# Kernel tuning notes

Measured on AMD Instinct MI355X. Metric: run time of the kernel, lower is better.

Reference implementation:

```python
import jax, jax.numpy as jnp
import numpy as np

B = 131072
D_IN = 256
HID = 256
N_EXPERTS = 4
N_IN_CAPS = 1
CAP_DIM = 16
BN_EPS = 1e-5


def setup_inputs() -> dict:
    key = jax.random.key(0)
    ks = jax.random.split(key, 8)
    return {
        "x": jax.random.normal(ks[0], (B, D_IN), dtype=jnp.float32),
        "fc_w": jax.random.normal(ks[1], (HID, D_IN), dtype=jnp.float32) * (1.0 / np.sqrt(D_IN)),
        "fc_b": jax.random.normal(ks[2], (HID,), dtype=jnp.float32) * 0.01,
        "bn_gamma": jnp.ones((HID,), dtype=jnp.float32),
        "bn_beta": jnp.zeros((HID,), dtype=jnp.float32),
        "W_caps": jax.random.normal(ks[3], (N_EXPERTS, N_IN_CAPS, HID, CAP_DIM), dtype=jnp.float32),
        "out_w": jax.random.normal(ks[4], (N_EXPERTS, CAP_DIM), dtype=jnp.float32) * (1.0 / np.sqrt(CAP_DIM)),
        "out_b": jax.random.normal(ks[5], (N_EXPERTS,), dtype=jnp.float32) * 0.01,
    }


def _squash(v):
    # norm/(1+norm^2) * v/(norm+1e-8), norm over last axis
    norm = jnp.linalg.norm(v, axis=-1, keepdims=True)
    return (norm / (1.0 + norm * norm)) * (v / (norm + 1e-8))


def reference(x, fc_w, fc_b, bn_gamma, bn_beta, W_caps, out_w, out_b):
    # Linear 256->256
    h = x @ fc_w.T + fc_b                                   # [B, HID]
    # BatchNorm1d (training-mode batch statistics, biased variance)
    mean = jnp.mean(h, axis=0)
    var = jnp.mean(jnp.square(h - mean), axis=0)
    h = (h - mean) * jax.lax.rsqrt(var + BN_EPS) * bn_gamma + bn_beta
    h = jax.nn.relu(h)
    # Capsule layer: input capsules [B, N_IN, HID]
    x_cap = h[:, None, :]                                   # [B, 1, HID]
    # u[b,e,n,o] = sum_d x_cap[b,n,d] * W_caps[e,n,d,o]
    u = jnp.einsum('bnd,endo->beno', x_cap, W_caps)         # [B, E, 1, 16]
    u_hat = _squash(u)
    # dynamic routing, 3 iterations
    b = jnp.zeros((x.shape[0], N_EXPERTS, N_IN_CAPS), dtype=h.dtype)
    v = None
    for i in range(3):
        c = jax.nn.softmax(b, axis=1)                       # over experts
        s = jnp.sum(c[..., None] * u_hat, axis=2)           # [B, E, 16]
        v = _squash(s)
        if i < 2:
            b = b + jnp.sum(u_hat * v[:, :, None, :], axis=-1)
    # output head + softmax
    logits = jnp.einsum('bec,kc->bek', v, out_w) + out_b    # [B, E, E]
    return jax.nn.softmax(logits, axis=-1)
```

## Files before the change

### kernel.cpp

```cpp
#include <hip/hip_runtime.h>
#include <hip/hip_bf16.h>


#define BATCH   131072
#define INV_B   (1.0f / 131072.0f)

typedef __attribute__((ext_vector_type(8))) short  short8;
typedef __attribute__((ext_vector_type(4))) float  f32x4;

__device__ __forceinline__ unsigned bf16_rn(float f) {
    unsigned u = __float_as_uint(f);
    return (u + 0x7fffu + ((u >> 16) & 1u)) >> 16;
}

__device__ __forceinline__ unsigned pack2bf(float a, float b) {
    union { __hip_bfloat16 b; ushort u; } ca, cb;
    ca.b = __float2bfloat16(a);
    cb.b = __float2bfloat16(b);
    return (unsigned)ca.u | ((unsigned)cb.u << 16);
}

__device__ __forceinline__ void split8(const float* v, uint4& hi, uint4& lo) {
    unsigned hb[8], lb[8];
#pragma unroll
    for (int j = 0; j < 8; ++j) {
        union { __hip_bfloat16 b; ushort u; } ch, cl;
        ch.b = __float2bfloat16(v[j]);
        float res = v[j] - __bfloat162float(ch.b);
        cl.b = __float2bfloat16(res);
        hb[j] = ch.u;
        lb[j] = cl.u;
    }
    hi = make_uint4(hb[0] | (hb[1] << 16), hb[2] | (hb[3] << 16),
                    hb[4] | (hb[5] << 16), hb[6] | (hb[7] << 16));
    lo = make_uint4(lb[0] | (lb[1] << 16), lb[2] | (lb[3] << 16),
                    lb[4] | (lb[5] << 16), lb[6] | (lb[7] << 16));
}

__global__ void k_prep(const float* __restrict__ w, ushort* __restrict__ wsp,
                       float* __restrict__ gsum, float* __restrict__ gsq)
{
    if (blockIdx.x == 0) { gsum[threadIdx.x] = 0.f; gsq[threadIdx.x] = 0.f; }
    const int cid = (int)blockIdx.x * 256 + threadIdx.x;
    const int j   = cid >> 5;
    const int ks  = (cid >> 2) & 7;
    const int c   = cid & 3;
    const float* wp = w + j * 256 + ks * 32 + c * 8;
    float4 v0 = *(const float4*)(wp);
    float4 v1 = *(const float4*)(wp + 4);
    float va[8] = {v0.x, v0.y, v0.z, v0.w, v1.x, v1.y, v1.z, v1.w};
    uint4 hi, lo;
    split8(va, hi, lo);
    const int slot = (c + (j >> 1)) & 3;
    *(uint4*)&wsp[ks * 8192 + j * 32 + slot * 8]         = hi;
    *(uint4*)&wsp[65536 + ks * 8192 + j * 32 + slot * 8] = lo;
}

__global__ __launch_bounds__(256, 4) void k_gemm(
    const float* __restrict__ x, const ushort* __restrict__ wsp,
    const float* __restrict__ bias, ushort* __restrict__ h,
    float* __restrict__ gsum, float* __restrict__ gsq)
{
    __shared__ ushort POOL[16896];
    __shared__ float  csum[128];
    __shared__ float  csq[128];

    const int t   = threadIdx.x;
    const int wid = t >> 6;
    const int l   = t & 63;
    const int wm  = wid >> 1;
    const int wn  = wid & 1;
    const int g   = l >> 4;
    const int lc  = l & 15;

    const int wg = ((int)blockIdx.x & 7) * 256 + ((int)blockIdx.x >> 3);
    const int bm = (wg >> 1) * 128;
    const int bn = (wg & 1) * 128;

    if (t < 128) { csum[t] = 0.f; csq[t] = 0.f; }

    f32x4 acc[4][4];
#pragma unroll
    for (int mi = 0; mi < 4; ++mi)
#pragma unroll
        for (int ni = 0; ni < 4; ++ni)
            acc[mi][ni] = (f32x4){0.f, 0.f, 0.f, 0.f};

    float bb[4];
#pragma unroll
    for (int ni = 0; ni < 4; ++ni)
        bb[ni] = bias[bn + wn * 64 + ni * 16 + lc];

    const int arow = t >> 3;
    const int ac8  = t & 7;
    const int acp  = ac8 >> 1;
    const int ahf  = ac8 & 1;

    const int isLo    = wid >> 1;
    const int halfsel = wid & 1;

#pragma unroll 1
    for (int ks = 0; ks < 8; ++ks) {
        __syncthreads();

        {
            const char* src = (const char*)(wsp + isLo * 65536 + ks * 8192
                                            + bn * 32 + halfsel * 2048);
            char* dst = (char*)&POOL[4096 + isLo * 4096 + halfsel * 2048];
#pragma unroll
            for (int i = 0; i < 4; ++i) {
                __builtin_amdgcn_global_load_lds(
                    (const __attribute__((address_space(1))) unsigned*)(src + i * 1024 + l * 16),
                    (__attribute__((address_space(3))) unsigned*)(dst + i * 1024),
                    16, 0, 0);
            }
        }

#pragma unroll
        for (int p = 0; p < 4; ++p) {
            const int r = p * 32 + arow;
            const float* ap = x + (size_t)(bm + r) * 256 + ks * 32 + ac8 * 4;
            float4 v = *(const float4*)ap;
            uint2 pk;
            pk.x = pack2bf(v.x, v.y);
            pk.y = pack2bf(v.z, v.w);
            const int s = (acp + (r >> 1)) & 3;
            *(uint2*)&POOL[r * 32 + s * 8 + ahf * 4] = pk;
        }
        __syncthreads();

        short8 ahfrag[4];
#pragma unroll
        for (int mi = 0; mi < 4; ++mi) {
            const int row = wm * 64 + mi * 16 + lc;
            const int off = row * 32 + ((g + (row >> 1)) & 3) * 8;
            ahfrag[mi] = *(const short8*)&POOL[off];
        }
#pragma unroll
        for (int ni = 0; ni < 4; ++ni) {
            const int col = wn * 64 + ni * 16 + lc;
            const int off = col * 32 + ((g + (col >> 1)) & 3) * 8;
            short8 bhf = *(const short8*)&POOL[4096 + off];
            short8 blf = *(const short8*)&POOL[8192 + off];
#pragma unroll
            for (int mi = 0; mi < 4; ++mi) {
                acc[mi][ni] = __builtin_amdgcn_mfma_f32_16x16x32_bf16(
                    ahfrag[mi], bhf, acc[mi][ni], 0, 0, 0);
                acc[mi][ni] = __builtin_amdgcn_mfma_f32_16x16x32_bf16(
                    ahfrag[mi], blf, acc[mi][ni], 0, 0, 0);
            }
        }
    }

    __syncthreads();

    float lsum[4] = {0.f, 0.f, 0.f, 0.f};
    float lsq[4]  = {0.f, 0.f, 0.f, 0.f};

#pragma unroll
    for (int mi = 0; mi < 4; ++mi)
#pragma unroll
        for (int ni = 0; ni < 4; ++ni) {
            const int colL = wn * 64 + ni * 16 + lc;
#pragma unroll
            for (int reg = 0; reg < 4; ++reg) {
                const int rowL = wm * 64 + mi * 16 + g * 4 + reg;
                float hv = acc[mi][ni][reg] + bb[ni];
                unsigned hb = bf16_rn(hv);
                float hq = __uint_as_float(hb << 16);
                POOL[rowL * 132 + colL] = (ushort)hb;
                lsum[ni] += hq;
                lsq[ni]   = fmaf(hq, hq, lsq[ni]);
            }
        }
    __syncthreads();

#pragma unroll
    for (int p = 0; p < 8; ++p) {
        const int r   = p * 16 + (t >> 4);
        const int c16 = t & 15;
        short8 vv = *(const short8*)&POOL[r * 132 + c16 * 8];
        *(short8*)(h + (size_t)(bm + r) * 256 + bn + c16 * 8) = vv;
    }

#pragma unroll
    for (int ni = 0; ni < 4; ++ni) {
        lsum[ni] += __shfl_xor(lsum[ni], 16);
        lsum[ni] += __shfl_xor(lsum[ni], 32);
        lsq[ni]  += __shfl_xor(lsq[ni], 16);
        lsq[ni]  += __shfl_xor(lsq[ni], 32);
    }
    if (l < 16) {
#pragma unroll
        for (int ni = 0; ni < 4; ++ni) {
            atomicAdd(&csum[wn * 64 + ni * 16 + lc], lsum[ni]);
            atomicAdd(&csq[wn * 64 + ni * 16 + lc],  lsq[ni]);
        }
    }
    __syncthreads();
    if (t < 128) {
        atomicAdd(&gsum[bn + t], csum[t]);
        atomicAdd(&gsq[bn + t],  csq[t]);
    }
}

__global__ __launch_bounds__(256) void k_fuse(
    const ushort* __restrict__ h,
    const float* __restrict__ gsum, const float* __restrict__ gsq,
    const float* __restrict__ gamma, const float* __restrict__ beta,
    const float* __restrict__ wc, const float* __restrict__ ow_g,
    const float* __restrict__ ob_g, float* __restrict__ out)
{
    __shared__ ushort Hh[32 * 256];
    __shared__ ushort Hl[32 * 256];
    __shared__ float  us[64 * 68];
    __shared__ float  ows[64];
    __shared__ float  abs_[512];

    const int t   = threadIdx.x;
    const int wid = t >> 6;
    const int l   = t & 63;
    const int g   = l >> 4;
    const int lc  = l & 15;

    {
        float mean = gsum[t] * INV_B;
        float var  = gsq[t] * INV_B - mean * mean;
        float rstd = rsqrtf(var + 1e-5f);
        float a = gamma[t] * rstd;
        abs_[t]       = a;
        abs_[256 + t] = beta[t] - mean * a;
    }
    if (t < 64) ows[t] = ow_g[t];

    short8 afh[8], afl[8];
#pragma unroll
    for (int ks = 0; ks < 8; ++ks) {
        union { ushort u16[8]; short8 v; } ph, pl;
#pragma unroll
        for (int j = 0; j < 8; ++j) {
            const int d = ks * 32 + g * 8 + j;
            float wv = wc[wid * 4096 + d * 16 + lc];
            unsigned hh = bf16_rn(wv);
            float res = wv - __uint_as_float(hh << 16);
            ph.u16[j] = (ushort)hh;
            pl.u16[j] = (ushort)bf16_rn(res);
        }
        afh[ks] = ph.v;
        afl[ks] = pl.v;
    }
    __syncthreads();

    const int c8 = (t & 31) * 8;
    float a_[8], cj[8];
    {
        float4 x0 = *(const float4*)(abs_ + c8);
        float4 x1 = *(const float4*)(abs_ + c8 + 4);
        float4 y0 = *(const float4*)(abs_ + 256 + c8);
        float4 y1 = *(const float4*)(abs_ + 256 + c8 + 4);
        a_[0]=x0.x; a_[1]=x0.y; a_[2]=x0.z; a_[3]=x0.w;
        a_[4]=x1.x; a_[5]=x1.y; a_[6]=x1.z; a_[7]=x1.w;
        cj[0]=y0.x; cj[1]=y0.y; cj[2]=y0.z; cj[3]=y0.w;
        cj[4]=y1.x; cj[5]=y1.y; cj[6]=y1.z; cj[7]=y1.w;
    }

    const int rowBase = (int)blockIdx.x * 64;

#pragma unroll
    for (int sub = 0; sub < 2; ++sub) {
        const int row0 = rowBase + sub * 32;

        __syncthreads();

#pragma unroll
        for (int it = 0; it < 4; ++it) {
            const int r = it * 8 + (t >> 5);
            const ushort* hp = h + (size_t)(row0 + r) * 256 + c8;
            short8 hraw = *(const short8*)hp;
            float hv[8];
#pragma unroll
            for (int j = 0; j < 8; ++j) {
                unsigned ub = (unsigned)(ushort)hraw[j];
                hv[j] = __uint_as_float(ub << 16);
                hv[j] = fmaxf(fmaf(hv[j], a_[j], cj[j]), 0.f);
            }
            uint4 hi, lo;
            split8(hv, hi, lo);
            const int slot = (t & 31) ^ (r & 7);
            *(uint4*)&Hh[r * 256 + slot * 8] = hi;
            *(uint4*)&Hl[r * 256 + slot * 8] = lo;
        }
        __syncthreads();

        f32x4 acc0 = (f32x4){0.f,0.f,0.f,0.f};
        f32x4 acc1 = (f32x4){0.f,0.f,0.f,0.f};
#pragma unroll
        for (int ks = 0; ks < 8; ++ks) {
            {
                const int row  = lc;
                const int slot = (ks * 4 + g) ^ (row & 7);
                short8 bh = *(const short8*)&Hh[row * 256 + slot * 8];
                short8 bl = *(const short8*)&Hl[row * 256 + slot * 8];
                acc0 = __builtin_amdgcn_mfma_f32_16x16x32_bf16(afh[ks], bh, acc0, 0,0,0);
                acc0 = __builtin_amdgcn_mfma_f32_16x16x32_bf16(afh[ks], bl, acc0, 0,0,0);
                acc0 = __builtin_amdgcn_mfma_f32_16x16x32_bf16(afl[ks], bh, acc0, 0,0,0);
            }
            {
                const int row  = 16 + lc;
                const int slot = (ks * 4 + g) ^ (row & 7);
                short8 bh = *(const short8*)&Hh[row * 256 + slot * 8];
                short8 bl = *(const short8*)&Hl[row * 256 + slot * 8];
                acc1 = __builtin_amdgcn_mfma_f32_16x16x32_bf16(afh[ks], bh, acc1, 0,0,0);
                acc1 = __builtin_amdgcn_mfma_f32_16x16x32_bf16(afh[ks], bl, acc1, 0,0,0);
                acc1 = __builtin_amdgcn_mfma_f32_16x16x32_bf16(afl[ks], bh, acc1, 0,0,0);
            }
        }
        {
            const int r0 = sub * 32 + lc;
            *(float4*)&us[r0 * 68 + wid * 16 + g * 4] =
                make_float4(acc0[0], acc0[1], acc0[2], acc0[3]);
            *(float4*)&us[(r0 + 16) * 68 + wid * 16 + g * 4] =
                make_float4(acc1[0], acc1[1], acc1[2], acc1[3]);
        }
    }
    __syncthreads();

    const int row_l = wid * 16 + lc;
    float u[16];
#pragma unroll
    for (int q = 0; q < 4; ++q) {
        float4 v4 = *(const float4*)&us[row_l * 68 + g * 16 + q * 4];
        u[q*4+0] = v4.x; u[q*4+1] = v4.y; u[q*4+2] = v4.z; u[q*4+3] = v4.w;
    }

    float n2 = 0.f;
#pragma unroll
    for (int o = 0; o < 16; ++o) n2 = fmaf(u[o], u[o], n2);
    const float nrm = sqrtf(n2);
    const float sc  = nrm / ((1.f + n2) * (nrm + 1e-8f));
    const float nh2 = sc * sc * n2;
    const float nh  = sc * nrm;

    float tk[4];
#pragma unroll
    for (int k = 0; k < 4; ++k) {
        float s = 0.f;
#pragma unroll
        for (int q = 0; q < 4; ++q) {
            float4 w4 = *(const float4*)&ows[k * 16 + q * 4];
            s = fmaf(u[q*4+0], w4.x, s);
            s = fmaf(u[q*4+1], w4.y, s);
            s = fmaf(u[q*4+2], w4.z, s);
            s = fmaf(u[q*4+3], w4.w, s);
        }
        tk[k] = s;
    }

    float b = 0.f, alc = 0.f;
#pragma unroll
    for (int it3 = 0; it3 < 3; ++it3) {
        float bmax = fmaxf(b, __shfl_xor(b, 16));
        bmax = fmaxf(bmax, __shfl_xor(bmax, 32));
        float eb = __expf(b - bmax);
        float es = eb + __shfl_xor(eb, 16);
        es += __shfl_xor(es, 32);
        float c = eb / es;
        float ns  = c * nh;
        float ns2 = c * c * nh2;
        float av  = ns / ((1.f + ns2) * (ns + 1e-8f));
        alc = av * c;
        if (it3 < 2) b += alc * nh2;
    }

    const float vs = alc * sc;
    float p0 = fmaf(vs, tk[0], ob_g[0]);
    float p1 = fmaf(vs, tk[1], ob_g[1]);
    float p2 = fmaf(vs, tk[2], ob_g[2]);
    float p3 = fmaf(vs, tk[3], ob_g[3]);
    float mx = fmaxf(fmaxf(p0, p1), fmaxf(p2, p3));
    float e0 = __expf(p0 - mx), e1 = __expf(p1 - mx);
    float e2 = __expf(p2 - mx), e3 = __expf(p3 - mx);
    float inv = 1.f / (e0 + e1 + e2 + e3);
    *(float4*)&out[(size_t)(rowBase + row_l) * 16 + g * 4] =
        make_float4(e0 * inv, e1 * inv, e2 * inv, e3 * inv);
}

extern "C" void kernel_launch(void* const* d_in, const int* in_sizes, int n_in,
                              void* d_out, int out_size, void* d_ws, size_t ws_size,
                              hipStream_t stream)
{
    const float* x     = (const float*)d_in[0];
    const float* fc_w  = (const float*)d_in[1];
    const float* fc_b  = (const float*)d_in[2];
    const float* gamma = (const float*)d_in[3];
    const float* beta  = (const float*)d_in[4];
    const float* wc    = (const float*)d_in[5];
    const float* ow    = (const float*)d_in[6];
    const float* ob    = (const float*)d_in[7];
    float* out = (float*)d_out;

    float*  gsum = (float*)d_ws;
    float*  gsq  = gsum + 256;
    ushort* h    = (ushort*)((char*)d_ws + 4096);

    ushort* wsp = (ushort*)d_out;

    k_prep <<<dim3(32),   dim3(256), 0, stream>>>(fc_w, wsp, gsum, gsq);
    k_gemm <<<dim3(2048), dim3(256), 0, stream>>>(x, wsp, fc_b, h, gsum, gsq);
    k_fuse <<<dim3(2048), dim3(256), 0, stream>>>(h, gsum, gsq, gamma, beta,
                                                  wc, ow, ob, out);
}
```

Before: 89.39 us.

## Double-buffer GEMM LDS tiles and prefetch next K-slice during MFMA

Splits the shared-memory pool into two buffers and restructures the K loop so the next slice's x loads (into registers) and weight global_load_lds transfers are issued before the current slice's MFMA work. Explicit vmcnt/lgkmcnt waits and a single s_barrier per iteration replace the two __syncthreads, so memory latency can be hidden behind compute. In exchange the kernel uses more LDS and registers, and launch_bounds drops from 4 to 3 blocks per SM, which lowers occupancy. The hand-counted vmcnt values also depend on how many loads the compiler actually emits, so miscounted waits would be a correctness risk.

```diff
diff --git a/kernel.cpp b/kernel.cpp
--- a/kernel.cpp
+++ b/kernel.cpp
@@ -56,12 +56,12 @@
     *(uint4*)&wsp[65536 + ks * 8192 + j * 32 + slot * 8] = lo;
 }
 
-__global__ __launch_bounds__(256, 4) void k_gemm(
+__global__ __launch_bounds__(256, 3) void k_gemm(
     const float* __restrict__ x, const ushort* __restrict__ wsp,
     const float* __restrict__ bias, ushort* __restrict__ h,
     float* __restrict__ gsum, float* __restrict__ gsq)
 {
-    __shared__ ushort POOL[16896];
+    __shared__ ushort POOL[2][12288];
     __shared__ float  csum[128];
     __shared__ float  csq[128];
 
@@ -96,63 +96,106 @@
     const int acp  = ac8 >> 1;
     const int ahf  = ac8 & 1;
 
-    const int isLo    = wid >> 1;
-    const int halfsel = wid & 1;
-
+    const char* srcBh0 = (const char*)(wsp + (size_t)(bn + wn * 64) * 32);
+    const char* srcBl0 = (const char*)(wsp + 65536 + (size_t)(bn + wn * 64) * 32);
+
+#define LOAD_A(KS, VA)                                                        \
+    _Pragma("unroll")                                                         \
+    for (int p_ = 0; p_ < 4; ++p_) {                                          \
+        const int r_ = p_ * 32 + arow;                                        \
+        VA[p_] = *(const float4*)(x + (size_t)(bm + r_) * 256 + (KS) * 32 + ac8 * 4); \
+    }
+
+#define STAGE_B(KS, BUF)                                                      \
+    {                                                                         \
+        const char* sh_ = srcBh0 + (KS) * 16384;                              \
+        const char* sl_ = srcBl0 + (KS) * 16384;                              \
+        char* dh_ = (char*)&POOL[BUF][4096] + wn * 4096;                      \
+        char* dl_ = (char*)&POOL[BUF][8192] + wn * 4096;                      \
+        _Pragma("unroll")                                                     \
+        for (int i_ = 0; i_ < 4; ++i_) {                                      \
+            __builtin_amdgcn_global_load_lds(                                 \
+                (const __attribute__((address_space(1))) unsigned*)(sh_ + i_ * 1024 + l * 16), \
+                (__attribute__((address_space(3))) unsigned*)(dh_ + i_ * 1024), 16, 0, 0); \
+            __builtin_amdgcn_global_load_lds(                                 \
+                (const __attribute__((address_space(1))) unsigned*)(sl_ + i_ * 1024 + l * 16), \
+                (__attribute__((address_space(3))) unsigned*)(dl_ + i_ * 1024), 16, 0, 0); \
+        }                                                                     \
+    }
+
+#define WRITE_A(BUF, VA)                                                      \
+    _Pragma("unroll")                                                         \
+    for (int p_ = 0; p_ < 4; ++p_) {                                          \
+        const int r_ = p_ * 32 + arow;                                        \
+        uint2 pk_;                                                            \
+        pk_.x = pack2bf(VA[p_].x, VA[p_].y);                                  \
+        pk_.y = pack2bf(VA[p_].z, VA[p_].w);                                  \
+        const int s_ = (acp + (r_ >> 1)) & 3;                                 \
+        *(uint2*)&POOL[BUF][r_ * 32 + s_ * 8 + ahf * 4] = pk_;                \
+    }
+
+    float4 va[4];
+    LOAD_A(0, va)
+    __builtin_amdgcn_sched_barrier(0);
+    STAGE_B(0, 0)
+    asm volatile("s_waitcnt vmcnt(8)" ::: "memory");
+    __builtin_amdgcn_sched_barrier(0);
+    WRITE_A(0, va)
+    asm volatile("s_waitcnt lgkmcnt(0)" ::: "memory");
+    __builtin_amdgcn_s_barrier();
+
+    int cur = 0;
 #pragma unroll 1
     for (int ks = 0; ks < 8; ++ks) {
-        __syncthreads();
+        if (ks < 7) {
+            LOAD_A(ks + 1, va)
+            __builtin_amdgcn_sched_barrier(0);
+            STAGE_B(ks + 1, cur ^ 1)
+            asm volatile("s_waitcnt vmcnt(12)" ::: "memory");
+        } else {
+            asm volatile("s_waitcnt vmcnt(0)" ::: "memory");
+        }
+        __builtin_amdgcn_sched_barrier(0);
 
         {
-            const char* src = (const char*)(wsp + isLo * 65536 + ks * 8192
-                                            + bn * 32 + halfsel * 2048);
-            char* dst = (char*)&POOL[4096 + isLo * 4096 + halfsel * 2048];
-#pragma unroll
-            for (int i = 0; i < 4; ++i) {
-                __builtin_amdgcn_global_load_lds(
-                    (const __attribute__((address_space(1))) unsigned*)(src + i * 1024 + l * 16),
-                    (__attribute__((address_space(3))) unsigned*)(dst + i * 1024),
-                    16, 0, 0);
-            }
-        }
-
-#pragma unroll
-        for (int p = 0; p < 4; ++p) {
-            const int r = p * 32 + arow;
-            const float* ap = x + (size_t)(bm + r) * 256 + ks * 32 + ac8 * 4;
-            float4 v = *(const float4*)ap;
-            uint2 pk;
-            pk.x = pack2bf(v.x, v.y);
-            pk.y = pack2bf(v.z, v.w);
-            const int s = (acp + (r >> 1)) & 3;
-            *(uint2*)&POOL[r * 32 + s * 8 + ahf * 4] = pk;
-        }
-        __syncthreads();
-
-        short8 ahfrag[4];
-#pragma unroll
-        for (int mi = 0; mi < 4; ++mi) {
-            const int row = wm * 64 + mi * 16 + lc;
-            const int off = row * 32 + ((g + (row >> 1)) & 3) * 8;
-            ahfrag[mi] = *(const short8*)&POOL[off];
-        }
-#pragma unroll
-        for (int ni = 0; ni < 4; ++ni) {
-            const int col = wn * 64 + ni * 16 + lc;
-            const int off = col * 32 + ((g + (col >> 1)) & 3) * 8;
-            short8 bhf = *(const short8*)&POOL[4096 + off];
-            short8 blf = *(const short8*)&POOL[8192 + off];
+            short8 ahfrag[4];
 #pragma unroll
             for (int mi = 0; mi < 4; ++mi) {
-                acc[mi][ni] = __builtin_amdgcn_mfma_f32_16x16x32_bf16(
-                    ahfrag[mi], bhf, acc[mi][ni], 0, 0, 0);
-                acc[mi][ni] = __builtin_amdgcn_mfma_f32_16x16x32_bf16(
-                    ahfrag[mi], blf, acc[mi][ni], 0, 0, 0);
-            }
-        }
-    }
+                const int row = wm * 64 + mi * 16 + lc;
+                const int off = row * 32 + ((g + (row >> 1)) & 3) * 8;
+                ahfrag[mi] = *(const short8*)&POOL[cur][off];
+            }
+#pragma unroll
+            for (int ni = 0; ni < 4; ++ni) {
+                const int col = wn * 64 + ni * 16 + lc;
+                const int off = col * 32 + ((g + (col >> 1)) & 3) * 8;
+                short8 bhf = *(const short8*)&POOL[cur][4096 + off];
+                short8 blf = *(const short8*)&POOL[cur][8192 + off];
+#pragma unroll
+                for (int mi = 0; mi < 4; ++mi) {
+                    acc[mi][ni] = __builtin_amdgcn_mfma_f32_16x16x32_bf16(
+                        ahfrag[mi], bhf, acc[mi][ni], 0, 0, 0);
+                    acc[mi][ni] = __builtin_amdgcn_mfma_f32_16x16x32_bf16(
+                        ahfrag[mi], blf, acc[mi][ni], 0, 0, 0);
+                }
+            }
+        }
+
+        if (ks < 7) {
+            asm volatile("s_waitcnt vmcnt(8)" ::: "memory");
+            __builtin_amdgcn_sched_barrier(0);
+            WRITE_A(cur ^ 1, va)
+            asm volatile("s_waitcnt lgkmcnt(0)" ::: "memory");
+            __builtin_amdgcn_s_barrier();
+        }
+        cur ^= 1;
+    }
+#undef LOAD_A
+#undef STAGE_B
+#undef WRITE_A
 
     __syncthreads();
+    ushort* HT = (ushort*)POOL;
 
     float lsum[4] = {0.f, 0.f, 0.f, 0.f};
     float lsq[4]  = {0.f, 0.f, 0.f, 0.f};
@@ -168,7 +211,7 @@
                 float hv = acc[mi][ni][reg] + bb[ni];
                 unsigned hb = bf16_rn(hv);
                 float hq = __uint_as_float(hb << 16);
-                POOL[rowL * 132 + colL] = (ushort)hb;
+                HT[rowL * 132 + colL] = (ushort)hb;
                 lsum[ni] += hq;
                 lsq[ni]   = fmaf(hq, hq, lsq[ni]);
             }
@@ -179,7 +222,7 @@
     for (int p = 0; p < 8; ++p) {
         const int r   = p * 16 + (t >> 4);
         const int c16 = t & 15;
-        short8 vv = *(const short8*)&POOL[r * 132 + c16 * 8];
+        short8 vv = *(const short8*)&HT[r * 132 + c16 * 8];
         *(short8*)(h + (size_t)(bm + r) * 256 + bn + c16 * 8) = vv;
     }
 
```

Measured after the change: 103.8 us. +16.1%, slower.
